# Kernel tuning notes

Measured on AMD Instinct MI355X. Metric: run time of the kernel, lower is better.

The kernel has to match this reference:

```python
import jax, jax.numpy as jnp
import numpy as np

B = 32768

def setup_inputs() -> dict:
    key = jax.random.key(0)
    ks = jax.random.split(key, 6)
    x = jax.random.normal(ks[0], (B, 1, 28, 28), dtype=jnp.float32)
    conv_w = jax.random.normal(ks[1], (4, 1, 2, 2), dtype=jnp.float32) * 0.5   # Conv2d(1,4,2,2) OIHW
    conv_b = jax.random.normal(ks[2], (4,), dtype=jnp.float32) * 0.1
    q_w = jax.random.normal(ks[3], (4, 4), dtype=jnp.float32) * 0.5            # Linear(4,4,bias=False), (out,in)
    lin_w = jax.random.normal(ks[4], (10, 1568), dtype=jnp.float32) * 0.02     # Linear(1568,10), (out,in)
    lin_b = jax.random.normal(ks[5], (10,), dtype=jnp.float32) * 0.02
    return {"x": x, "conv_w": conv_w, "conv_b": conv_b, "q_w": q_w, "lin_w": lin_w, "lin_b": lin_b}

def reference(x, conv_w, conv_b, q_w, lin_w, lin_b):
    b = x.shape[0]
    # conv branch: (B,1,28,28) -> (B,4,14,14)
    conv = jax.lax.conv_general_dilated(
        x, conv_w, window_strides=(2, 2), padding='VALID',
        dimension_numbers=('NCHW', 'OIHW', 'NCHW')) + conv_b[None, :, None, None]
    cls_feat = conv.reshape(b, -1)  # (B,784)
    # quantum branch: all 196 non-overlapping 2x2 patches in loop (r,c) order,
    # each flattened row-major to 4 values, then one batched 4x4 linear.
    img = x.reshape(b, 28, 28)
    patches = img.reshape(b, 14, 2, 14, 2).transpose(0, 1, 3, 2, 4).reshape(b, 196, 4)
    qfeat = jnp.einsum('bpi,oi->bpo', patches, q_w).reshape(b, 196 * 4)  # (B,784)
    combined = jnp.concatenate([cls_feat, qfeat], axis=1)  # (B,1568)
    logits = combined @ lin_w.T + lin_b
    return jax.nn.log_softmax(logits, axis=-1)
```

## Files before the change

### kernel.cpp

```cpp
#include <hip/hip_runtime.h>
#include <math.h>

#define NOUT   10
#define ROWLEN 784
#define WTOT   (NOUT*ROWLEN)

__global__ __launch_bounds__(256)
void quanv_prep(const float* __restrict__ conv_w,
                const float* __restrict__ conv_b,
                const float* __restrict__ q_w,
                const float* __restrict__ lin_w,
                const float* __restrict__ lin_b,
                float* __restrict__ W)
{
    const int t = threadIdx.x;

    for (int idx = blockIdx.x * 256 + t; idx < WTOT; idx += gridDim.x * 256) {
        const int o = idx / ROWLEN;
        const int j = idx - o * ROWLEN;
        const int h = j / 28, w = j - h * 28;
        const int p = (h >> 1) * 14 + (w >> 1);
        const int k = (h & 1) * 2 + (w & 1);
        float s = 0.f;
        #pragma unroll
        for (int c = 0; c < 4; ++c)
            s += conv_w[c * 4 + k] * lin_w[o * 1568 + c * 196 + p];
        #pragma unroll
        for (int q = 0; q < 4; ++q)
            s += q_w[q * 4 + k] * lin_w[o * 1568 + 784 + p * 4 + q];
        W[idx] = s;
    }

    if (blockIdx.x == 0) {
        __shared__ float rs[40];
        const int lane = t & 7;
        for (int pair = t >> 3; pair < 40; pair += 32) {
            const int o = pair >> 2, c = pair & 3;
            const float* base = lin_w + o * 1568 + c * 196;
            float s = 0.f;
            #pragma unroll
            for (int p = 0; p < 196; p += 8) {
                const int pp = p + lane;
                if (pp < 196) s += base[pp];
            }
            s += __shfl_xor(s, 1);
            s += __shfl_xor(s, 2);
            s += __shfl_xor(s, 4);
            if (lane == 0) rs[pair] = s;
        }
        __syncthreads();
        if (t < NOUT) {
            float s = lin_b[t];
            #pragma unroll
            for (int c = 0; c < 4; ++c) s += conv_b[c] * rs[t * 4 + c];
            W[WTOT + t] = s;
        }
    }
}

__global__ __launch_bounds__(256, 4)
void quanv_main(const float* __restrict__ x,
                const float* __restrict__ Wg,
                float* __restrict__ out)
{
    __shared__ float Wl[WTOT];
    __shared__ float bias[NOUT];

    {
        const float4* __restrict__ src = (const float4*)Wg;
        float4* dst = (float4*)Wl;
        #pragma unroll
        for (int i = 0; i < 8; ++i) {
            const int idx = threadIdx.x + 256 * i;
            if (idx < WTOT / 4) dst[idx] = src[idx];
        }
        if (threadIdx.x < NOUT) bias[threadIdx.x] = Wg[WTOT + threadIdx.x];
    }
    __syncthreads();

    const int t  = threadIdx.x;
    const int l  = t & 15;
    const int g  = t >> 4;
    const int r0 = blockIdx.x * 32 + 2 * g;

    const float* __restrict__ xr0 = x + (size_t)r0 * ROWLEN;
    const float* __restrict__ xr1 = xr0 + ROWLEN;

    float acc0[NOUT], acc1[NOUT];
    #pragma unroll
    for (int o = 0; o < NOUT; ++o) { acc0[o] = 0.f; acc1[o] = 0.f; }

    float4 pa0 = *(const float4*)(xr0 + 4 * l);
    float4 pb0 = *(const float4*)(xr1 + 4 * l);
    float4 pa1 = *(const float4*)(xr0 + 4 * l + 64);
    float4 pb1 = *(const float4*)(xr1 + 4 * l + 64);

    #pragma unroll
    for (int i = 0; i < 12; ++i) {
        float4 a, b;
        if ((i & 1) == 0) { a = pa0; b = pb0; } else { a = pa1; b = pb1; }

        const int ni = i + 2;
        if (ni < 12) {
            const int nfo = 4 * l + 64 * ni;
            if ((i & 1) == 0) {
                pa0 = *(const float4*)(xr0 + nfo);
                pb0 = *(const float4*)(xr1 + nfo);
            } else {
                pa1 = *(const float4*)(xr0 + nfo);
                pb1 = *(const float4*)(xr1 + nfo);
            }
        } else if (ni == 12) {
            const int tfo = 768 + 4 * (l & 3);
            pa0 = *(const float4*)(xr0 + tfo);
            pb0 = *(const float4*)(xr1 + tfo);
        }

        const int fo = 4 * l + 64 * i;
        #pragma unroll
        for (int o = 0; o < NOUT; ++o) {
            const float4 wv = *(const float4*)&Wl[o * ROWLEN + fo];
            acc0[o] = fmaf(a.x, wv.x, fmaf(a.y, wv.y, fmaf(a.z, wv.z, fmaf(a.w, wv.w, acc0[o]))));
            acc1[o] = fmaf(b.x, wv.x, fmaf(b.y, wv.y, fmaf(b.z, wv.z, fmaf(b.w, wv.w, acc1[o]))));
        }
    }
    if (l < 4) {
        const int fo = 768 + 4 * l;
        #pragma unroll
        for (int o = 0; o < NOUT; ++o) {
            const float4 wv = *(const float4*)&Wl[o * ROWLEN + fo];
            acc0[o] = fmaf(pa0.x, wv.x, fmaf(pa0.y, wv.y, fmaf(pa0.z, wv.z, fmaf(pa0.w, wv.w, acc0[o]))));
            acc1[o] = fmaf(pb0.x, wv.x, fmaf(pb0.y, wv.y, fmaf(pb0.z, wv.z, fmaf(pb0.w, wv.w, acc1[o]))));
        }
    }

    #pragma unroll
    for (int o = 0; o < NOUT; ++o) {
        acc0[o] += __shfl_xor(acc0[o], 1);
        acc0[o] += __shfl_xor(acc0[o], 2);
        acc0[o] += __shfl_xor(acc0[o], 4);
        acc0[o] += __shfl_xor(acc0[o], 8);
        acc1[o] += __shfl_xor(acc1[o], 1);
        acc1[o] += __shfl_xor(acc1[o], 2);
        acc1[o] += __shfl_xor(acc1[o], 4);
        acc1[o] += __shfl_xor(acc1[o], 8);
    }

    float lg0[NOUT], lg1[NOUT];
    float m0 = -1e30f, m1 = -1e30f;
    #pragma unroll
    for (int o = 0; o < NOUT; ++o) {
        lg0[o] = acc0[o] + bias[o]; m0 = fmaxf(m0, lg0[o]);
        lg1[o] = acc1[o] + bias[o]; m1 = fmaxf(m1, lg1[o]);
    }
    float s0 = 0.f, s1 = 0.f;
    #pragma unroll
    for (int o = 0; o < NOUT; ++o) {
        s0 += expf(lg0[o] - m0);
        s1 += expf(lg1[o] - m1);
    }
    const float lse0 = m0 + logf(s0);
    const float lse1 = m1 + logf(s1);

    if (l < NOUT) {
        float v0 = lg0[0], v1 = lg1[0];
        #pragma unroll
        for (int o = 1; o < NOUT; ++o) {
            v0 = (l == o) ? lg0[o] : v0;
            v1 = (l == o) ? lg1[o] : v1;
        }
        out[(size_t)r0 * NOUT + l]       = v0 - lse0;
        out[(size_t)(r0 + 1) * NOUT + l] = v1 - lse1;
    }
}

extern "C" void kernel_launch(void* const* d_in, const int* in_sizes, int n_in,
                              void* d_out, int out_size, void* d_ws, size_t ws_size,
                              hipStream_t stream) {
    const float* x      = (const float*)d_in[0];
    const float* conv_w = (const float*)d_in[1];
    const float* conv_b = (const float*)d_in[2];
    const float* q_w    = (const float*)d_in[3];
    const float* lin_w  = (const float*)d_in[4];
    const float* lin_b  = (const float*)d_in[5];
    float* out = (float*)d_out;
    float* W   = (float*)d_ws;

    const int rows = in_sizes[0] / ROWLEN;

    quanv_prep<<<31, 256, 0, stream>>>(conv_w, conv_b, q_w, lin_w, lin_b, W);
    quanv_main<<<rows / 32, 256, 0, stream>>>(x, W, out);
}
```

Baseline: 32.23 us.

## Register-block 4 rows x 5 outputs per thread group and prefetch x before weight staging

Each 16-lane group now computes 4 rows for half of the 10 outputs instead of 2 rows for all 10. This halves the shared-memory weight reads per FMA, and the two half-output groups are combined with a cross-group shuffle before log-softmax. The first x loads are also issued before the shared-memory weight copy and barrier so that global latency overlaps staging. In exchange, more x float4 registers stay live at once, which may pressure occupancy.

```diff
diff --git a/kernel.cpp b/kernel.cpp
--- a/kernel.cpp
+++ b/kernel.cpp
@@ -66,111 +66,135 @@
     __shared__ float Wl[WTOT];
     __shared__ float bias[NOUT];
 
+    const int t     = threadIdx.x;
+    const int lane  = t & 63;
+    const int wv    = t >> 6;
+    const int l     = lane & 15;
+    const int grp   = lane >> 4;
+    const int pair  = grp >> 1;
+    const int gp    = grp & 1;
+    const int obase = gp * 5;
+    const int r0    = blockIdx.x * 32 + wv * 8 + pair * 4;
+
+    const float* __restrict__ xr = x + (size_t)r0 * ROWLEN;
+
+    float4 px0[4], px1[4];
+    #pragma unroll
+    for (int r = 0; r < 4; ++r) {
+        px0[r] = *(const float4*)(xr + r * ROWLEN + 4 * l);
+        px1[r] = *(const float4*)(xr + r * ROWLEN + 4 * l + 64);
+    }
+
     {
         const float4* __restrict__ src = (const float4*)Wg;
         float4* dst = (float4*)Wl;
         #pragma unroll
         for (int i = 0; i < 8; ++i) {
-            const int idx = threadIdx.x + 256 * i;
+            const int idx = t + 256 * i;
             if (idx < WTOT / 4) dst[idx] = src[idx];
         }
-        if (threadIdx.x < NOUT) bias[threadIdx.x] = Wg[WTOT + threadIdx.x];
+        if (t < NOUT) bias[t] = Wg[WTOT + t];
     }
     __syncthreads();
 
-    const int t  = threadIdx.x;
-    const int l  = t & 15;
-    const int g  = t >> 4;
-    const int r0 = blockIdx.x * 32 + 2 * g;
-
-    const float* __restrict__ xr0 = x + (size_t)r0 * ROWLEN;
-    const float* __restrict__ xr1 = xr0 + ROWLEN;
-
-    float acc0[NOUT], acc1[NOUT];
-    #pragma unroll
-    for (int o = 0; o < NOUT; ++o) { acc0[o] = 0.f; acc1[o] = 0.f; }
-
-    float4 pa0 = *(const float4*)(xr0 + 4 * l);
-    float4 pb0 = *(const float4*)(xr1 + 4 * l);
-    float4 pa1 = *(const float4*)(xr0 + 4 * l + 64);
-    float4 pb1 = *(const float4*)(xr1 + 4 * l + 64);
+    float acc[4][5];
+    #pragma unroll
+    for (int r = 0; r < 4; ++r)
+        #pragma unroll
+        for (int o = 0; o < 5; ++o) acc[r][o] = 0.f;
+
+    const int wb = obase * ROWLEN;
 
     #pragma unroll
     for (int i = 0; i < 12; ++i) {
-        float4 a, b;
-        if ((i & 1) == 0) { a = pa0; b = pb0; } else { a = pa1; b = pb1; }
+        float4 cur[4];
+        #pragma unroll
+        for (int r = 0; r < 4; ++r) cur[r] = ((i & 1) == 0) ? px0[r] : px1[r];
 
         const int ni = i + 2;
         if (ni < 12) {
             const int nfo = 4 * l + 64 * ni;
-            if ((i & 1) == 0) {
-                pa0 = *(const float4*)(xr0 + nfo);
-                pb0 = *(const float4*)(xr1 + nfo);
-            } else {
-                pa1 = *(const float4*)(xr0 + nfo);
-                pb1 = *(const float4*)(xr1 + nfo);
+            #pragma unroll
+            for (int r = 0; r < 4; ++r) {
+                const float4 v = *(const float4*)(xr + r * ROWLEN + nfo);
+                if ((i & 1) == 0) px0[r] = v; else px1[r] = v;
             }
         } else if (ni == 12) {
             const int tfo = 768 + 4 * (l & 3);
-            pa0 = *(const float4*)(xr0 + tfo);
-            pb0 = *(const float4*)(xr1 + tfo);
+            #pragma unroll
+            for (int r = 0; r < 4; ++r)
+                px0[r] = *(const float4*)(xr + r * ROWLEN + tfo);
         }
 
         const int fo = 4 * l + 64 * i;
         #pragma unroll
-        for (int o = 0; o < NOUT; ++o) {
-            const float4 wv = *(const float4*)&Wl[o * ROWLEN + fo];
-            acc0[o] = fmaf(a.x, wv.x, fmaf(a.y, wv.y, fmaf(a.z, wv.z, fmaf(a.w, wv.w, acc0[o]))));
-            acc1[o] = fmaf(b.x, wv.x, fmaf(b.y, wv.y, fmaf(b.z, wv.z, fmaf(b.w, wv.w, acc1[o]))));
+        for (int o = 0; o < 5; ++o) {
+            const float4 w4 = *(const float4*)&Wl[wb + o * ROWLEN + fo];
+            #pragma unroll
+            for (int r = 0; r < 4; ++r)
+                acc[r][o] = fmaf(cur[r].x, w4.x, fmaf(cur[r].y, w4.y,
+                            fmaf(cur[r].z, w4.z, fmaf(cur[r].w, w4.w, acc[r][o]))));
         }
     }
     if (l < 4) {
         const int fo = 768 + 4 * l;
         #pragma unroll
-        for (int o = 0; o < NOUT; ++o) {
-            const float4 wv = *(const float4*)&Wl[o * ROWLEN + fo];
-            acc0[o] = fmaf(pa0.x, wv.x, fmaf(pa0.y, wv.y, fmaf(pa0.z, wv.z, fmaf(pa0.w, wv.w, acc0[o]))));
-            acc1[o] = fmaf(pb0.x, wv.x, fmaf(pb0.y, wv.y, fmaf(pb0.z, wv.z, fmaf(pb0.w, wv.w, acc1[o]))));
-        }
-    }
-
-    #pragma unroll
-    for (int o = 0; o < NOUT; ++o) {
-        acc0[o] += __shfl_xor(acc0[o], 1);
-        acc0[o] += __shfl_xor(acc0[o], 2);
-        acc0[o] += __shfl_xor(acc0[o], 4);
-        acc0[o] += __shfl_xor(acc0[o], 8);
-        acc1[o] += __shfl_xor(acc1[o], 1);
-        acc1[o] += __shfl_xor(acc1[o], 2);
-        acc1[o] += __shfl_xor(acc1[o], 4);
-        acc1[o] += __shfl_xor(acc1[o], 8);
-    }
-
-    float lg0[NOUT], lg1[NOUT];
-    float m0 = -1e30f, m1 = -1e30f;
-    #pragma unroll
-    for (int o = 0; o < NOUT; ++o) {
-        lg0[o] = acc0[o] + bias[o]; m0 = fmaxf(m0, lg0[o]);
-        lg1[o] = acc1[o] + bias[o]; m1 = fmaxf(m1, lg1[o]);
-    }
-    float s0 = 0.f, s1 = 0.f;
-    #pragma unroll
-    for (int o = 0; o < NOUT; ++o) {
-        s0 += expf(lg0[o] - m0);
-        s1 += expf(lg1[o] - m1);
-    }
-    const float lse0 = m0 + logf(s0);
-    const float lse1 = m1 + logf(s1);
+        for (int o = 0; o < 5; ++o) {
+            const float4 w4 = *(const float4*)&Wl[wb + o * ROWLEN + fo];
+            #pragma unroll
+            for (int r = 0; r < 4; ++r)
+                acc[r][o] = fmaf(px0[r].x, w4.x, fmaf(px0[r].y, w4.y,
+                            fmaf(px0[r].z, w4.z, fmaf(px0[r].w, w4.w, acc[r][o]))));
+        }
+    }
+
+    #pragma unroll
+    for (int r = 0; r < 4; ++r)
+        #pragma unroll
+        for (int o = 0; o < 5; ++o) {
+            acc[r][o] += __shfl_xor(acc[r][o], 1);
+            acc[r][o] += __shfl_xor(acc[r][o], 2);
+            acc[r][o] += __shfl_xor(acc[r][o], 4);
+            acc[r][o] += __shfl_xor(acc[r][o], 8);
+        }
+
+    float own[4][5], part[4][5];
+    #pragma unroll
+    for (int r = 0; r < 4; ++r)
+        #pragma unroll
+        for (int o = 0; o < 5; ++o) {
+            own[r][o]  = acc[r][o] + bias[obase + o];
+            part[r][o] = __shfl_xor(own[r][o], 16);
+        }
+
+    float lgA[10], lgB[10];
+    #pragma unroll
+    for (int o = 0; o < 5; ++o) {
+        lgA[o]     = gp ? part[2][o] : own[0][o];
+        lgA[o + 5] = gp ? own[2][o]  : part[0][o];
+        lgB[o]     = gp ? part[3][o] : own[1][o];
+        lgB[o + 5] = gp ? own[3][o]  : part[1][o];
+    }
+
+    float mA = -1e30f, mB = -1e30f;
+    #pragma unroll
+    for (int o = 0; o < 10; ++o) { mA = fmaxf(mA, lgA[o]); mB = fmaxf(mB, lgB[o]); }
+    float sA = 0.f, sB = 0.f;
+    #pragma unroll
+    for (int o = 0; o < 10; ++o) { sA += expf(lgA[o] - mA); sB += expf(lgB[o] - mB); }
+    const float lseA = mA + logf(sA);
+    const float lseB = mB + logf(sB);
 
     if (l < NOUT) {
-        float v0 = lg0[0], v1 = lg1[0];
-        #pragma unroll
-        for (int o = 1; o < NOUT; ++o) {
-            v0 = (l == o) ? lg0[o] : v0;
-            v1 = (l == o) ? lg1[o] : v1;
-        }
-        out[(size_t)r0 * NOUT + l]       = v0 - lse0;
-        out[(size_t)(r0 + 1) * NOUT + l] = v1 - lse1;
+        float vA = lgA[0], vB = lgB[0];
+        #pragma unroll
+        for (int o = 1; o < 10; ++o) {
+            vA = (l == o) ? lgA[o] : vA;
+            vB = (l == o) ? lgB[o] : vB;
+        }
+        const int rA = r0 + 2 * gp;
+        out[(size_t)rA * NOUT + l]       = vA - lseA;
+        out[(size_t)(rA + 1) * NOUT + l] = vB - lseB;
     }
 }
 
```

After: 31.90 us. No clear change (-1.0%).
